# Kernel optimization log

Measured on AMD Instinct MI355X. Metric: run time of the kernel, lower is better.

## Reference

```python
import jax, jax.numpy as jnp
import numpy as np

N_CODES = 1024
DIM = 64
COMMITMENT = 0.25


def setup_inputs() -> dict:
    key = jax.random.key(0)
    k1, k2 = jax.random.split(key)
    z = jax.random.normal(k1, (32, DIM, 64, 64), dtype=jnp.float32)
    # nn.Embedding weight initialized uniform(-1/n_codes, 1/n_codes)
    codebook = jax.random.uniform(
        k2, (N_CODES, DIM), dtype=jnp.float32,
        minval=-1.0 / N_CODES, maxval=1.0 / N_CODES)
    return {"z": z, "codebook": codebook}


def reference(z, codebook):
    B, C, H, W = z.shape
    # (B,C,H,W) -> (B*H*W, C)
    z_flat = jnp.transpose(z, (0, 2, 3, 1)).reshape(-1, C)
    # squared L2 distances via expansion: |z|^2 + |e|^2 - 2 z.e
    dists = (
        jnp.sum(z_flat ** 2, axis=1, keepdims=True)
        + jnp.sum(codebook ** 2, axis=1)
        - 2.0 * z_flat @ codebook.T
    )  # [N, n_codes]
    indices = jnp.argmin(dists, axis=1)  # [N]
    z_q = jnp.transpose(codebook[indices].reshape(B, H, W, C), (0, 3, 1, 2))
    commit_loss = jnp.mean((jax.lax.stop_gradient(z_q) - z) ** 2)
    codebook_loss = jnp.mean((z_q - jax.lax.stop_gradient(z)) ** 2)
    vq_loss = codebook_loss + COMMITMENT * commit_loss
    z_q_st = z + jax.lax.stop_gradient(z_q - z)  # straight-through
    return (z_q_st, vq_loss)
```

## Files before the change

### kernel.cpp

```cpp
#include <hip/hip_runtime.h>


constexpr int DIM    = 64;
constexpr int NCODES = 1024;
constexpr int HWSZ   = 4096;
constexpr int NPOS   = 131072;
constexpr int BLOCK  = 512;
constexpr int TPW    = 4;
constexpr int PPB    = 512;
constexpr int GRID   = NPOS / PPB;

typedef __bf16 bf16x8 __attribute__((ext_vector_type(8)));
typedef unsigned short ushort8t __attribute__((ext_vector_type(8)));
typedef float f32x4 __attribute__((ext_vector_type(4)));

__device__ __forceinline__ unsigned short f2bf(float f) {
    unsigned u = __float_as_uint(f);
    u += 0x7fffu + ((u >> 16) & 1u);
    return (unsigned short)(u >> 16);
}

__global__ __launch_bounds__(256) void vq_prep(const float* __restrict__ cb,
                                               float* __restrict__ cinitT,
                                               unsigned short* __restrict__ cbbf) {
    int m = blockIdx.x * 256 + threadIdx.x;
    int j = m >> 3, g = m & 7;
    const float4* src = (const float4*)(cb + (size_t)j * DIM + g * 8);
    float4 v0 = src[0], v1 = src[1];
    ushort8t u;
    u[0] = f2bf(v0.x); u[1] = f2bf(v0.y); u[2] = f2bf(v0.z); u[3] = f2bf(v0.w);
    u[4] = f2bf(v1.x); u[5] = f2bf(v1.y); u[6] = f2bf(v1.z); u[7] = f2bf(v1.w);
    float ps = v0.x * v0.x + v0.y * v0.y + v0.z * v0.z + v0.w * v0.w
             + v1.x * v1.x + v1.y * v1.y + v1.z * v1.z + v1.w * v1.w;
    ps += __shfl_xor(ps, 1, 64);
    ps += __shfl_xor(ps, 2, 64);
    ps += __shfl_xor(ps, 4, 64);
    if (g == 0) cinitT[(j & 15) * 64 + (j >> 4)] = fmaf(-0.5f, ps, 1.0f);
    *(ushort8t*)(cbbf + ((size_t)j * 8 + (g ^ (j & 7))) * 8) = u;
}

__global__ __launch_bounds__(BLOCK, 2) void vq_main(const float* __restrict__ z,
                                                    const float* __restrict__ cinitT,
                                                    const unsigned short* __restrict__ cbbf,
                                                    float* __restrict__ out,
                                                    float* __restrict__ wsblk) {
    __shared__ __align__(16) unsigned short cb_lds[NCODES * DIM];
    __shared__ int   bj_lds[PPB];
    __shared__ float ls_lds[BLOCK / 64];

    const int tid  = threadIdx.x;
    const int w    = tid >> 6;
    const int lane = tid & 63;
    const int q    = lane >> 4;
    const int r    = lane & 15;
    const int p0   = blockIdx.x * PPB;
    const int b    = p0 >> 12;
    const int hwb  = p0 & 4095;

#pragma unroll
    for (int it = 0; it < (NCODES * DIM * 2) / (BLOCK * 16); it++) {
        int off = (it * BLOCK + tid) * 16;
        __builtin_amdgcn_global_load_lds(
            (const __attribute__((address_space(1))) void*)((const char*)cbbf + off),
            (__attribute__((address_space(3))) void*)((char*)cb_lds + off), 16, 0, 0);
    }

    bf16x8 afrag[TPW][2];
    float  zsq[TPW];
    const float* zb = z + (size_t)b * DIM * HWSZ + hwb + w * 64 + r;
#pragma unroll
    for (int t = 0; t < TPW; t++) {
        float sq = 0.f;
#pragma unroll
        for (int h = 0; h < 2; h++) {
            ushort8t u;
#pragma unroll
            for (int i = 0; i < 8; i++) {
                float v = zb[(size_t)(h * 32 + q * 8 + i) * HWSZ + t * 16];
                sq = fmaf(v, v, sq);
                u[i] = f2bf(v);
            }
            afrag[t][h] = __builtin_bit_cast(bf16x8, u);
        }
        sq += __shfl_xor(sq, 16, 64);
        sq += __shfl_xor(sq, 32, 64);
        zsq[t] = sq;
    }

    unsigned best[TPW][4];
#pragma unroll
    for (int t = 0; t < TPW; t++)
#pragma unroll
        for (int g = 0; g < 4; g++) best[t][g] = 0u;

    __syncthreads();

    bf16x8 B[2][2];
    float4 ci[2];
#pragma unroll
    for (int s = 0; s < 2; s++) {
        int row = s * 16 + r;
#pragma unroll
        for (int h = 0; h < 2; h++) {
            int grp = (h * 4 + q) ^ (row & 7);
            B[s][h] = *(const bf16x8*)&cb_lds[(size_t)row * 64 + grp * 8];
        }
    }
    ci[0] = *(const float4*)(cinitT + r * 64 + 0);
    ci[1] = *(const float4*)(cinitT + r * 64 + 4);

    const f32x4 zero4 = {0.f, 0.f, 0.f, 0.f};

    for (int G2 = 0; G2 < 8; G2++) {
#pragma unroll
        for (int gg = 0; gg < 2; gg++) {
#pragma unroll
            for (int e = 0; e < 4; e++) {
                const int jt   = G2 * 8 + gg * 4 + e;
                const int slot = e & 1;
                const int row  = jt * 16 + r;
                const float    cin   = ci[gg][e];
                const unsigned inv_j = (unsigned)(1023 - row);
#pragma unroll
                for (int t = 0; t < TPW; t++) {
                    f32x4 acc = __builtin_amdgcn_mfma_f32_16x16x32_bf16(
                        afrag[t][0], B[slot][0], zero4, 0, 0, 0);
                    acc = __builtin_amdgcn_mfma_f32_16x16x32_bf16(
                        afrag[t][1], B[slot][1], acc, 0, 0, 0);
#pragma unroll
                    for (int g = 0; g < 4; g++) {
                        unsigned bits = (__float_as_uint(cin + acc[g]) & ~1023u) | inv_j;
                        best[t][g] = best[t][g] > bits ? best[t][g] : bits;
                    }
                }
                const int rown = ((jt + 2) & 63) * 16 + r;
#pragma unroll
                for (int h = 0; h < 2; h++) {
                    int grp = (h * 4 + q) ^ (rown & 7);
                    B[slot][h] = *(const bf16x8*)&cb_lds[(size_t)rown * 64 + grp * 8];
                }
            }
            ci[gg] = *(const float4*)(cinitT + r * 64 + ((G2 * 2 + gg + 2) & 15) * 4);
        }
    }

#pragma unroll
    for (int t = 0; t < TPW; t++)
#pragma unroll
        for (int g = 0; g < 4; g++) {
            unsigned v = best[t][g];
#pragma unroll
            for (int off = 1; off < 16; off <<= 1) {
                unsigned v2 = __shfl_xor((int)v, off, 64);
                v = v > v2 ? v : v2;
            }
            best[t][g] = v;
        }

    float lsum = 0.f;
    if (q == (r >> 2)) {
        int g = r & 3;
#pragma unroll
        for (int t = 0; t < TPW; t++) {
            unsigned v = best[t][0];
            v = (g == 1) ? best[t][1] : v;
            v = (g == 2) ? best[t][2] : v;
            v = (g == 3) ? best[t][3] : v;
            bj_lds[w * 64 + t * 16 + r] = 1023 - (int)(v & 1023u);
            lsum += zsq[t] + 2.f - 2.f * __uint_as_float(v);
        }
    }
#pragma unroll
    for (int off = 32; off > 0; off >>= 1) lsum += __shfl_down(lsum, off, 64);
    if (lane == 0) ls_lds[w] = lsum;
    __syncthreads();
    if (tid == 0) {
        float s = 0.f;
#pragma unroll
        for (int i = 0; i < BLOCK / 64; i++) s += ls_lds[i];
        wsblk[blockIdx.x] = s;
    }

    int myj = bj_lds[tid];
    int rc  = myj & 7;
    float* ob = out + (size_t)b * DIM * HWSZ + hwb + tid;
#pragma unroll
    for (int g = 0; g < 8; g++) {
        int gs = g ^ rc;
        ushort8t u = *(const ushort8t*)&cb_lds[(size_t)myj * 64 + gs * 8];
#pragma unroll
        for (int i = 0; i < 8; i++) {
            ob[(size_t)(g * 8 + i) * HWSZ] = __uint_as_float(((unsigned)u[i]) << 16);
        }
    }
}

__global__ void vq_fin(const float* __restrict__ wsblk, float* __restrict__ out_loss) {
    int t = threadIdx.x;
    float s = wsblk[t] + wsblk[t + 64] + wsblk[t + 128] + wsblk[t + 192];
#pragma unroll
    for (int off = 32; off > 0; off >>= 1) s += __shfl_down(s, off, 64);
    if (t == 0) out_loss[0] = 1.25f * s / (float)((size_t)NPOS * DIM);
}

extern "C" void kernel_launch(void* const* d_in, const int* in_sizes, int n_in,
                              void* d_out, int out_size, void* d_ws, size_t ws_size,
                              hipStream_t stream) {
    const float* z  = (const float*)d_in[0];
    const float* cb = (const float*)d_in[1];
    float* out = (float*)d_out;

    float*          cinitT = (float*)d_ws;
    unsigned short* cbbf   = (unsigned short*)((char*)d_ws + 4096);
    float*          wsblk  = (float*)((char*)d_ws + 4096 + 131072);

    vq_prep<<<NCODES * 8 / 256, 256, 0, stream>>>(cb, cinitT, cbbf);
    vq_main<<<GRID, BLOCK, 0, stream>>>(z, cinitT, cbbf, out, wsblk);
    vq_fin<<<1, 64, 0, stream>>>(wsblk, out + (size_t)NPOS * DIM);
}
```

Measured before the change: 112.8 us.

## Switch distance GEMM and codebook storage from bf16 to scaled fp8

The codebook is quantized to fp8 with a ×512 scale, and the z fragments are converted to fp8. The distance search uses fp8 MFMA, with the codebook-norm term folded into the accumulator init. Halving the codebook's LDS footprint lets the kernel target four blocks per CU with half as many positions per block, and the output gather dequantizes from fp8. This trades argmin accuracy and z_q precision (fp8 has only 3 mantissa bits) for higher matrix throughput, more resident waves and less LDS traffic, so the outputs could fall outside tolerance.

After: 114.1 us. No clear change (+1.2%).

```diff
diff --git a/kernel.cpp b/kernel.cpp
--- a/kernel.cpp
+++ b/kernel.cpp
@@ -6,45 +6,53 @@
 constexpr int HWSZ   = 4096;
 constexpr int NPOS   = 131072;
 constexpr int BLOCK  = 512;
-constexpr int TPW    = 4;
-constexpr int PPB    = 512;
+constexpr int TPW    = 2;
+constexpr int PPB    = 256;
 constexpr int GRID   = NPOS / PPB;
 
-typedef __bf16 bf16x8 __attribute__((ext_vector_type(8)));
-typedef unsigned short ushort8t __attribute__((ext_vector_type(8)));
-typedef float f32x4 __attribute__((ext_vector_type(4)));
-
-__device__ __forceinline__ unsigned short f2bf(float f) {
-    unsigned u = __float_as_uint(f);
-    u += 0x7fffu + ((u >> 16) & 1u);
-    return (unsigned short)(u >> 16);
-}
+typedef float    f32x4  __attribute__((ext_vector_type(4)));
+typedef float    f32x2  __attribute__((ext_vector_type(2)));
+typedef unsigned uint2v __attribute__((ext_vector_type(2)));
 
 __global__ __launch_bounds__(256) void vq_prep(const float* __restrict__ cb,
                                                float* __restrict__ cinitT,
-                                               unsigned short* __restrict__ cbbf) {
-    int m = blockIdx.x * 256 + threadIdx.x;
-    int j = m >> 3, g = m & 7;
-    const float4* src = (const float4*)(cb + (size_t)j * DIM + g * 8);
-    float4 v0 = src[0], v1 = src[1];
-    ushort8t u;
-    u[0] = f2bf(v0.x); u[1] = f2bf(v0.y); u[2] = f2bf(v0.z); u[3] = f2bf(v0.w);
-    u[4] = f2bf(v1.x); u[5] = f2bf(v1.y); u[6] = f2bf(v1.z); u[7] = f2bf(v1.w);
-    float ps = v0.x * v0.x + v0.y * v0.y + v0.z * v0.z + v0.w * v0.w
-             + v1.x * v1.x + v1.y * v1.y + v1.z * v1.z + v1.w * v1.w;
-    ps += __shfl_xor(ps, 1, 64);
-    ps += __shfl_xor(ps, 2, 64);
-    ps += __shfl_xor(ps, 4, 64);
-    if (g == 0) cinitT[(j & 15) * 64 + (j >> 4)] = fmaf(-0.5f, ps, 1.0f);
-    *(ushort8t*)(cbbf + ((size_t)j * 8 + (g ^ (j & 7))) * 8) = u;
-}
-
-__global__ __launch_bounds__(BLOCK, 2) void vq_main(const float* __restrict__ z,
+                                               unsigned* __restrict__ cbq) {
+    int j = blockIdx.x * 256 + threadIdx.x;
+    const float4* src = (const float4*)(cb + (size_t)j * DIM);
+    unsigned words[16];
+    float nq = 0.f;
+#pragma unroll
+    for (int g8 = 0; g8 < 8; g8++) {
+        float4 v0 = src[g8 * 2], v1 = src[g8 * 2 + 1];
+        int lo = 0, hi = 0;
+        lo = __builtin_amdgcn_cvt_pk_fp8_f32(v0.x * 512.f, v0.y * 512.f, lo, 0);
+        lo = __builtin_amdgcn_cvt_pk_fp8_f32(v0.z * 512.f, v0.w * 512.f, lo, 1);
+        hi = __builtin_amdgcn_cvt_pk_fp8_f32(v1.x * 512.f, v1.y * 512.f, hi, 0);
+        hi = __builtin_amdgcn_cvt_pk_fp8_f32(v1.z * 512.f, v1.w * 512.f, hi, 1);
+        words[g8 * 2] = (unsigned)lo; words[g8 * 2 + 1] = (unsigned)hi;
+#pragma unroll
+        for (int m = 0; m < 2; m++) {
+            int wv = m ? hi : lo;
+            f32x2 d0 = __builtin_amdgcn_cvt_pk_f32_fp8(wv, 0);
+            f32x2 d1 = __builtin_amdgcn_cvt_pk_f32_fp8(wv, 1);
+            nq += d0[0] * d0[0] + d0[1] * d0[1] + d1[0] * d1[0] + d1[1] * d1[1];
+        }
+    }
+#pragma unroll
+    for (int g8 = 0; g8 < 8; g8++) {
+        int gs = g8 ^ (j & 7);
+        uint2v u = {words[g8 * 2], words[g8 * 2 + 1]};
+        *(uint2v*)(cbq + ((size_t)j * 8 + gs) * 2) = u;
+    }
+    cinitT[(j & 15) * 64 + (j >> 4)] = 8.f - nq * (1.f / 1024.f);
+}
+
+__global__ __launch_bounds__(BLOCK, 4) void vq_main(const float* __restrict__ z,
                                                     const float* __restrict__ cinitT,
-                                                    const unsigned short* __restrict__ cbbf,
+                                                    const unsigned* __restrict__ cbq,
                                                     float* __restrict__ out,
                                                     float* __restrict__ wsblk) {
-    __shared__ __align__(16) unsigned short cb_lds[NCODES * DIM];
+    __shared__ __align__(16) unsigned char cb_lds[NCODES * DIM];
     __shared__ int   bj_lds[PPB];
     __shared__ float ls_lds[BLOCK / 64];
 
@@ -58,29 +66,34 @@
     const int hwb  = p0 & 4095;
 
 #pragma unroll
-    for (int it = 0; it < (NCODES * DIM * 2) / (BLOCK * 16); it++) {
+    for (int it = 0; it < (NCODES * DIM) / (BLOCK * 16); it++) {
         int off = (it * BLOCK + tid) * 16;
         __builtin_amdgcn_global_load_lds(
-            (const __attribute__((address_space(1))) void*)((const char*)cbbf + off),
-            (__attribute__((address_space(3))) void*)((char*)cb_lds + off), 16, 0, 0);
-    }
-
-    bf16x8 afrag[TPW][2];
-    float  zsq[TPW];
-    const float* zb = z + (size_t)b * DIM * HWSZ + hwb + w * 64 + r;
+            (const __attribute__((address_space(1))) void*)((const char*)cbq + off),
+            (__attribute__((address_space(3))) void*)(cb_lds + off), 16, 0, 0);
+    }
+
+    long  afrag[TPW][2];
+    float zsq[TPW];
+    const float* zb = z + (size_t)b * DIM * HWSZ + hwb + w * 32 + r;
 #pragma unroll
     for (int t = 0; t < TPW; t++) {
         float sq = 0.f;
 #pragma unroll
         for (int h = 0; h < 2; h++) {
-            ushort8t u;
+            float v[8];
 #pragma unroll
             for (int i = 0; i < 8; i++) {
-                float v = zb[(size_t)(h * 32 + q * 8 + i) * HWSZ + t * 16];
-                sq = fmaf(v, v, sq);
-                u[i] = f2bf(v);
+                v[i] = zb[(size_t)(h * 32 + q * 8 + i) * HWSZ + t * 16];
+                sq = fmaf(v[i], v[i], sq);
             }
-            afrag[t][h] = __builtin_bit_cast(bf16x8, u);
+            int lo = 0, hi = 0;
+            lo = __builtin_amdgcn_cvt_pk_fp8_f32(v[0], v[1], lo, 0);
+            lo = __builtin_amdgcn_cvt_pk_fp8_f32(v[2], v[3], lo, 1);
+            hi = __builtin_amdgcn_cvt_pk_fp8_f32(v[4], v[5], hi, 0);
+            hi = __builtin_amdgcn_cvt_pk_fp8_f32(v[6], v[7], hi, 1);
+            uint2v u = {(unsigned)lo, (unsigned)hi};
+            afrag[t][h] = __builtin_bit_cast(long, u);
         }
         sq += __shfl_xor(sq, 16, 64);
         sq += __shfl_xor(sq, 32, 64);
@@ -95,21 +108,19 @@
 
     __syncthreads();
 
-    bf16x8 B[2][2];
+    uint2v B[2][2];
     float4 ci[2];
 #pragma unroll
     for (int s = 0; s < 2; s++) {
         int row = s * 16 + r;
 #pragma unroll
         for (int h = 0; h < 2; h++) {
-            int grp = (h * 4 + q) ^ (row & 7);
-            B[s][h] = *(const bf16x8*)&cb_lds[(size_t)row * 64 + grp * 8];
+            int gs = (h * 4 + q) ^ (row & 7);
+            B[s][h] = *(const uint2v*)&cb_lds[(size_t)row * 64 + gs * 8];
         }
     }
     ci[0] = *(const float4*)(cinitT + r * 64 + 0);
     ci[1] = *(const float4*)(cinitT + r * 64 + 4);
-
-    const f32x4 zero4 = {0.f, 0.f, 0.f, 0.f};
 
     for (int G2 = 0; G2 < 8; G2++) {
 #pragma unroll
@@ -119,25 +130,28 @@
                 const int jt   = G2 * 8 + gg * 4 + e;
                 const int slot = e & 1;
                 const int row  = jt * 16 + r;
-                const float    cin   = ci[gg][e];
+                const float cin = ci[gg][e];
                 const unsigned inv_j = (unsigned)(1023 - row);
+                f32x4 c0 = {cin, cin, cin, cin};
+                long b0 = __builtin_bit_cast(long, B[slot][0]);
+                long b1 = __builtin_bit_cast(long, B[slot][1]);
 #pragma unroll
                 for (int t = 0; t < TPW; t++) {
-                    f32x4 acc = __builtin_amdgcn_mfma_f32_16x16x32_bf16(
-                        afrag[t][0], B[slot][0], zero4, 0, 0, 0);
-                    acc = __builtin_amdgcn_mfma_f32_16x16x32_bf16(
-                        afrag[t][1], B[slot][1], acc, 0, 0, 0);
+                    f32x4 acc = __builtin_amdgcn_mfma_f32_16x16x32_fp8_fp8(
+                        afrag[t][0], b0, c0, 0, 0, 0);
+                    acc = __builtin_amdgcn_mfma_f32_16x16x32_fp8_fp8(
+                        afrag[t][1], b1, acc, 0, 0, 0);
 #pragma unroll
                     for (int g = 0; g < 4; g++) {
-                        unsigned bits = (__float_as_uint(cin + acc[g]) & ~1023u) | inv_j;
+                        unsigned bits = (__float_as_uint(acc[g]) & ~1023u) | inv_j;
                         best[t][g] = best[t][g] > bits ? best[t][g] : bits;
                     }
                 }
                 const int rown = ((jt + 2) & 63) * 16 + r;
 #pragma unroll
                 for (int h = 0; h < 2; h++) {
-                    int grp = (h * 4 + q) ^ (rown & 7);
-                    B[slot][h] = *(const bf16x8*)&cb_lds[(size_t)rown * 64 + grp * 8];
+                    int gs = (h * 4 + q) ^ (rown & 7);
+                    B[slot][h] = *(const uint2v*)&cb_lds[(size_t)rown * 64 + gs * 8];
                 }
             }
             ci[gg] = *(const float4*)(cinitT + r * 64 + ((G2 * 2 + gg + 2) & 15) * 4);
@@ -166,8 +180,8 @@
             v = (g == 1) ? best[t][1] : v;
             v = (g == 2) ? best[t][2] : v;
             v = (g == 3) ? best[t][3] : v;
-            bj_lds[w * 64 + t * 16 + r] = 1023 - (int)(v & 1023u);
-            lsum += zsq[t] + 2.f - 2.f * __uint_as_float(v);
+            bj_lds[w * 32 + t * 16 + r] = 1023 - (int)(v & 1023u);
+            lsum += zsq[t] + (8.f - __uint_as_float(v)) * (1.f / 256.f);
         }
     }
 #pragma unroll
@@ -181,23 +195,32 @@
         wsblk[blockIdx.x] = s;
     }
 
-    int myj = bj_lds[tid];
-    int rc  = myj & 7;
-    float* ob = out + (size_t)b * DIM * HWSZ + hwb + tid;
-#pragma unroll
-    for (int g = 0; g < 8; g++) {
-        int gs = g ^ rc;
-        ushort8t u = *(const ushort8t*)&cb_lds[(size_t)myj * 64 + gs * 8];
-#pragma unroll
-        for (int i = 0; i < 8; i++) {
-            ob[(size_t)(g * 8 + i) * HWSZ] = __uint_as_float(((unsigned)u[i]) << 16);
+    int posi = tid & 255;
+    int h32  = tid >> 8;
+    int myj  = bj_lds[posi];
+    float* ob = out + (size_t)b * DIM * HWSZ + (size_t)(h32 * 32) * HWSZ + hwb + posi;
+#pragma unroll
+    for (int gg = 0; gg < 4; gg++) {
+        int g8 = h32 * 4 + gg;
+        int gs = g8 ^ (myj & 7);
+        uint2v u = *(const uint2v*)&cb_lds[(size_t)myj * 64 + gs * 8];
+#pragma unroll
+        for (int m = 0; m < 2; m++) {
+            f32x2 d0 = __builtin_amdgcn_cvt_pk_f32_fp8((int)u[m], 0);
+            f32x2 d1 = __builtin_amdgcn_cvt_pk_f32_fp8((int)u[m], 1);
+            ob[(size_t)(gg * 8 + m * 4 + 0) * HWSZ] = d0[0] * (1.f / 512.f);
+            ob[(size_t)(gg * 8 + m * 4 + 1) * HWSZ] = d0[1] * (1.f / 512.f);
+            ob[(size_t)(gg * 8 + m * 4 + 2) * HWSZ] = d1[0] * (1.f / 512.f);
+            ob[(size_t)(gg * 8 + m * 4 + 3) * HWSZ] = d1[1] * (1.f / 512.f);
         }
     }
 }
 
 __global__ void vq_fin(const float* __restrict__ wsblk, float* __restrict__ out_loss) {
     int t = threadIdx.x;
-    float s = wsblk[t] + wsblk[t + 64] + wsblk[t + 128] + wsblk[t + 192];
+    float s = 0.f;
+#pragma unroll
+    for (int k = 0; k < GRID / 64; k++) s += wsblk[t + k * 64];
 #pragma unroll
     for (int off = 32; off > 0; off >>= 1) s += __shfl_down(s, off, 64);
     if (t == 0) out_loss[0] = 1.25f * s / (float)((size_t)NPOS * DIM);
@@ -210,11 +233,11 @@
     const float* cb = (const float*)d_in[1];
     float* out = (float*)d_out;
 
-    float*          cinitT = (float*)d_ws;
-    unsigned short* cbbf   = (unsigned short*)((char*)d_ws + 4096);
-    float*          wsblk  = (float*)((char*)d_ws + 4096 + 131072);
-
-    vq_prep<<<NCODES * 8 / 256, 256, 0, stream>>>(cb, cinitT, cbbf);
-    vq_main<<<GRID, BLOCK, 0, stream>>>(z, cinitT, cbbf, out, wsblk);
+    float*    cinitT = (float*)d_ws;
+    unsigned* cbq    = (unsigned*)((char*)d_ws + 4096);
+    float*    wsblk  = (float*)((char*)d_ws + 4096 + 65536);
+
+    vq_prep<<<NCODES / 256, 256, 0, stream>>>(cb, cinitT, cbq);
+    vq_main<<<GRID, BLOCK, 0, stream>>>(z, cinitT, cbq, out, wsblk);
     vq_fin<<<1, 64, 0, stream>>>(wsblk, out + (size_t)NPOS * DIM);
 }
```
